# Kernel tuning notes

Measured on AMD Instinct MI355X. Metric: run time of the kernel, lower is better.

Reference implementation:

```python
import jax, jax.numpy as jnp
import numpy as np

N_NODES = 50000
NEG_SLOPE = 0.2


def _gat_layer(h, W, al, ar, src, dst, residual):
    # h: [N, F_in], W: [F_in, H*D], al/ar: [H, D]
    N = h.shape[0]
    H, D = al.shape
    feat = (h @ W).reshape(N, H, D)                      # [N, H, D]
    el = jnp.sum(feat * al[None], axis=-1)               # [N, H]
    er = jnp.sum(feat * ar[None], axis=-1)               # [N, H]
    e = jax.nn.leaky_relu(el[src] + er[dst], NEG_SLOPE)  # [E, H]
    # edge softmax over incoming edges of each destination node
    m = jax.ops.segment_max(e, dst, num_segments=N)      # [N, H]
    m = jnp.where(jnp.isfinite(m), m, jnp.zeros_like(m))
    ex = jnp.exp(e - m[dst])                             # [E, H]
    den = jax.ops.segment_sum(ex, dst, num_segments=N)   # [N, H]
    a = ex / jnp.maximum(den[dst], jnp.asarray(1e-9, ex.dtype))
    msg = a[:, :, None] * feat[src]                      # [E, H, D]
    out = jax.ops.segment_sum(msg, dst, num_segments=N)  # [N, H, D]
    if residual:  # identity residual: in_feats == H*D
        out = out + h.reshape(N, H, D)
    out = jax.nn.relu(out)
    return out.reshape(N, H * D)


def setup_inputs() -> dict:
    key = jax.random.key(0)
    ks = jax.random.split(key, 12)
    N, E, F_IN, H, D = N_NODES, 400000, 256, 4, 64
    s = 1.0 / np.sqrt(F_IN)
    inp = {
        "x": jax.random.normal(ks[0], (N, F_IN), dtype=jnp.float32),
        "src": jax.random.randint(ks[1], (E,), 0, N, dtype=jnp.int32),
        "dst": jax.random.randint(ks[2], (E,), 0, N, dtype=jnp.int32),
    }
    for i in range(3):
        inp[f"W{i}"] = jax.random.normal(ks[3 + 3 * i], (F_IN, H * D), dtype=jnp.float32) * s
        inp[f"al{i}"] = jax.random.normal(ks[4 + 3 * i], (H, D), dtype=jnp.float32) * s
        inp[f"ar{i}"] = jax.random.normal(ks[5 + 3 * i], (H, D), dtype=jnp.float32) * s
    return inp


def reference(x, src, dst, W0, al0, ar0, W1, al1, ar1, W2, al2, ar2):
    h = _gat_layer(x, W0, al0, ar0, src, dst, residual=True)
    h = _gat_layer(h, W1, al1, ar1, src, dst, residual=True)
    h = _gat_layer(h, W2, al2, ar2, src, dst, residual=False)  # last_residual = encoding and residual = False
    return h
```

## Files before the change

### kernel.cpp

```cpp
#include <hip/hip_runtime.h>
#include <stdint.h>

typedef __bf16 bf16x8 __attribute__((ext_vector_type(8)));
typedef float f32x4 __attribute__((ext_vector_type(4)));

typedef __attribute__((address_space(1))) const unsigned int gu32;
typedef __attribute__((address_space(3))) unsigned int lu32;
__device__ __forceinline__ void gl_lds16(const void* g, void* l) {
  __builtin_amdgcn_global_load_lds((gu32*)g, (lu32*)l, 16, 0, 0);
}

__device__ __forceinline__ ushort f2bf(float f) {
  uint32_t u = __float_as_uint(f);
  u += 0x7FFFu + ((u >> 16) & 1u);
  return (ushort)(u >> 16);
}
__device__ __forceinline__ float bflo(uint u) { return __uint_as_float(u << 16); }
__device__ __forceinline__ float bfhi(uint u) { return __uint_as_float(u & 0xFFFF0000u); }

__global__ __launch_bounds__(256) void k_prep(const float* __restrict__ x,
                                              ushort* __restrict__ xb,
                                              const float* __restrict__ W0,
                                              const float* __restrict__ W1,
                                              const float* __restrict__ W2,
                                              ushort* __restrict__ T0,
                                              ushort* __restrict__ T1,
                                              ushort* __restrict__ T2,
                                              const int* __restrict__ dst,
                                              int* __restrict__ cnt,
                                              long totx, int E, int nb_cast) {
  __shared__ float t[64][65];
  int b = blockIdx.x;
  int tid = threadIdx.x;
  if (b < nb_cast) {
    long i = ((long)b * 256 + tid) * 8;
    if (i >= totx) return;
    float4 a = *(const float4*)(x + i);
    float4 c = *(const float4*)(x + i + 4);
    uint4 r;
    r.x = (uint)f2bf(a.x) | ((uint)f2bf(a.y) << 16);
    r.y = (uint)f2bf(a.z) | ((uint)f2bf(a.w) << 16);
    r.z = (uint)f2bf(c.x) | ((uint)f2bf(c.y) << 16);
    r.w = (uint)f2bf(c.z) | ((uint)f2bf(c.w) << 16);
    *(uint4*)(xb + i) = r;
  } else if (b < nb_cast + 48) {
    int idx = b - nb_cast;
    int z = idx >> 4, tile = idx & 15;
    const float* W = z == 0 ? W0 : (z == 1 ? W1 : W2);
    ushort* T = z == 0 ? T0 : (z == 1 ? T1 : T2);
    int r0 = (tile >> 2) * 64, c0 = (tile & 3) * 64;
    int tr = tid >> 4, tc = tid & 15;
#pragma unroll
    for (int i = 0; i < 4; ++i) {
      int r = tr + i * 16;
      float4 v = *(const float4*)(W + (size_t)(r0 + r) * 256 + c0 + tc * 4);
      t[r][tc * 4 + 0] = v.x; t[r][tc * 4 + 1] = v.y;
      t[r][tc * 4 + 2] = v.z; t[r][tc * 4 + 3] = v.w;
    }
    __syncthreads();
#pragma unroll
    for (int i = 0; i < 4; ++i) {
      int nn = tr + i * 16;
      int kk = tc * 4;
      ushort4 o;
      o.x = f2bf(t[kk + 0][nn]); o.y = f2bf(t[kk + 1][nn]);
      o.z = f2bf(t[kk + 2][nn]); o.w = f2bf(t[kk + 3][nn]);
      *(ushort4*)(T + (size_t)(c0 + nn) * 256 + r0 + kk) = o;
    }
  } else {
    int e = (b - nb_cast - 48) * 256 + tid;
    if (e < E) atomicAdd(&cnt[dst[e]], 1);
  }
}

__global__ __launch_bounds__(1024) void k_scan1(const int* __restrict__ cnt,
                                                int* __restrict__ rowptr,
                                                int* __restrict__ bsum, int N) {
  __shared__ int wsum[16];
  int tid = threadIdx.x, lane = tid & 63, wv = tid >> 6;
  int i = blockIdx.x * 1024 + tid;
  int v = (i < N) ? cnt[i] : 0;
  int x = v;
#pragma unroll
  for (int off = 1; off < 64; off <<= 1) {
    int y = __shfl_up(x, off);
    if (lane >= off) x += y;
  }
  if (lane == 63) wsum[wv] = x;
  __syncthreads();
  if (wv == 0) {
    int s = (lane < 16) ? wsum[lane] : 0;
#pragma unroll
    for (int off = 1; off < 16; off <<= 1) {
      int y = __shfl_up(s, off);
      if (lane >= off) s += y;
    }
    if (lane < 16) wsum[lane] = s;
  }
  __syncthreads();
  x += wv ? wsum[wv - 1] : 0;
  if (i < N) rowptr[i + 1] = x;
  if (tid == 0) bsum[blockIdx.x] = wsum[15];
}

__global__ void k_scan2(int* __restrict__ bsum, int G) {
  int lane = threadIdx.x & 63;
  int carry = 0;
  for (int base = 0; base < G; base += 64) {
    int b = base + lane;
    int v = (b < G) ? bsum[b] : 0;
    int x = v;
#pragma unroll
    for (int off = 1; off < 64; off <<= 1) {
      int y = __shfl_up(x, off);
      if (lane >= off) x += y;
    }
    if (b < G) bsum[b] = carry + x - v;
    carry += __shfl(x, 63);
  }
}

__global__ __launch_bounds__(1024) void k_scan3(int* __restrict__ rowptr,
                                                const int* __restrict__ bsum, int N) {
  int i = blockIdx.x * 1024 + threadIdx.x;
  if (i < N) rowptr[i + 1] += bsum[blockIdx.x];
  if (blockIdx.x == 0 && threadIdx.x == 0) rowptr[0] = 0;
}

__global__ __launch_bounds__(256) void k_scatter(const int* __restrict__ dst,
                                                 const int* __restrict__ src,
                                                 const int* __restrict__ rowptr,
                                                 int* __restrict__ fill,
                                                 int* __restrict__ esrc, int E) {
  int e = blockIdx.x * 256 + threadIdx.x;
  if (e < E) {
    int d = dst[e];
    int p = atomicAdd(&fill[d], 1);
    esrc[rowptr[d] + p] = src[e];
  }
}

#define BM 128
#define BN 128
#define BK 64

__global__ __launch_bounds__(512) void k_gemm_bf16(const ushort* __restrict__ A,
                                                   const ushort* __restrict__ Bt,
                                                   const float* __restrict__ al,
                                                   const float* __restrict__ ar,
                                                   ushort* __restrict__ C,
                                                   float* __restrict__ el,
                                                   float* __restrict__ er, int M) {
  __shared__ __align__(16) ushort As[2 * BM * BK];
  __shared__ __align__(16) ushort Bs[2 * BN * BK];
  const int K = 256, N = 256;
  int bn = blockIdx.x * BN;
  int bm = blockIdx.y * BM;
  int tid = threadIdx.x;
  int lane = tid & 63, wid = tid >> 6;
  int wr = wid >> 1;
  int wc = wid & 1;

  f32x4 acc[2][4];
#pragma unroll
  for (int mi = 0; mi < 2; ++mi)
#pragma unroll
    for (int ni = 0; ni < 4; ++ni) acc[mi][ni] = (f32x4){0.f, 0.f, 0.f, 0.f};

  auto stage = [&](int kt, int buf) {
#pragma unroll
    for (int i = 0; i < 2; ++i) {
      int r = i * 64 + (tid >> 3);
      int cs = (((tid & 7) ^ (r & 7)) << 3);
      int gr = bm + r;
      if (gr >= M) gr = M - 1;
      gl_lds16(A + (size_t)gr * K + kt + cs, As + buf * 8192 + i * 4096 + wid * 512);
      gl_lds16(Bt + (size_t)(bn + r) * K + kt + cs, Bs + buf * 8192 + i * 4096 + wid * 512);
    }
  };

  stage(0, 0);
  asm volatile("s_waitcnt vmcnt(0)" ::: "memory");
  __builtin_amdgcn_s_barrier();

  int swz = (lane & 7) << 3;
#pragma unroll
  for (int t = 0; t < 4; ++t) {
    int cur = t & 1;
    if (t < 3) stage((t + 1) * BK, cur ^ 1);
    const ushort* Ab = As + cur * 8192;
    const ushort* Bb = Bs + cur * 8192;
#pragma unroll
    for (int s = 0; s < 2; ++s) {
      bf16x8 af[2], bfr[4];
      int cc = s * 32 + (lane >> 4) * 8;
      int cs = cc ^ swz;
#pragma unroll
      for (int mi = 0; mi < 2; ++mi) {
        int r = wr * 32 + mi * 16 + (lane & 15);
        af[mi] = *(const bf16x8*)(Ab + r * BK + cs);
      }
#pragma unroll
      for (int ni = 0; ni < 4; ++ni) {
        int r = wc * 64 + ni * 16 + (lane & 15);
        bfr[ni] = *(const bf16x8*)(Bb + r * BK + cs);
      }
#pragma unroll
      for (int mi = 0; mi < 2; ++mi)
#pragma unroll
        for (int ni = 0; ni < 4; ++ni)
          acc[mi][ni] = __builtin_amdgcn_mfma_f32_16x16x32_bf16(af[mi], bfr[ni], acc[mi][ni], 0, 0, 0);
    }
    if (t < 3) {
      asm volatile("s_waitcnt vmcnt(0)" ::: "memory");
      __builtin_amdgcn_s_barrier();
    }
  }

#pragma unroll
  for (int mi = 0; mi < 2; ++mi) {
#pragma unroll
    for (int j = 0; j < 4; ++j) {
      int gr = bm + wr * 32 + mi * 16 + (lane >> 4) * 4 + j;
      if (gr < M) {
#pragma unroll
        for (int ni = 0; ni < 4; ++ni) {
          int gc = bn + wc * 64 + ni * 16 + (lane & 15);
          C[(size_t)gr * N + gc] = f2bf(acc[mi][ni][j]);
        }
      }
    }
  }

  int h = (bn >> 6) + wc;
  float alv[4], arv[4];
#pragma unroll
  for (int ni = 0; ni < 4; ++ni) {
    int d = ni * 16 + (lane & 15);
    alv[ni] = al[h * 64 + d];
    arv[ni] = ar[h * 64 + d];
  }
#pragma unroll
  for (int mi = 0; mi < 2; ++mi) {
#pragma unroll
    for (int j = 0; j < 4; ++j) {
      float pel = acc[mi][0][j] * alv[0] + acc[mi][1][j] * alv[1] +
                  acc[mi][2][j] * alv[2] + acc[mi][3][j] * alv[3];
      float per = acc[mi][0][j] * arv[0] + acc[mi][1][j] * arv[1] +
                  acc[mi][2][j] * arv[2] + acc[mi][3][j] * arv[3];
#pragma unroll
      for (int off = 8; off >= 1; off >>= 1) {
        pel += __shfl_xor(pel, off);
        per += __shfl_xor(per, off);
      }
      int gr = bm + wr * 32 + mi * 16 + (lane >> 4) * 4 + j;
      if ((lane & 15) == 0 && gr < M) {
        el[(size_t)gr * 4 + h] = pel;
        er[(size_t)gr * 4 + h] = per;
      }
    }
  }
}

#define CAP 128

__global__ __launch_bounds__(256) void k_agg(const ushort* __restrict__ feat,
                                             const float* __restrict__ el,
                                             const float* __restrict__ er,
                                             const int* __restrict__ rowptr,
                                             const int* __restrict__ esrc,
                                             const float* __restrict__ resid_f32,
                                             const ushort* __restrict__ resid_bf16,
                                             float* __restrict__ out_f32,
                                             ushort* __restrict__ out_bf16, int N) {
  __shared__ float lw[4][CAP * 4];
  int wv = threadIdx.x >> 6;
  int lane = threadIdx.x & 63;
  int n = blockIdx.x * 4 + wv;
  if (n >= N) return;
  int e0 = rowptr[n], e1 = rowptr[n + 1];
  int deg = e1 - e0;
  int h = lane >> 4, sub = lane & 15;
  float ern = er[(size_t)n * 4 + h];
  const ushort* fb = feat + (size_t)lane * 4;

  float a0 = 0.f, a1 = 0.f, a2 = 0.f, a3 = 0.f;
  float inv;

  if (deg <= 16) {
    int s_reg = 0;
    float v = -1e30f;
    if (sub < deg) {
      s_reg = esrc[e0 + sub];
      v = el[(size_t)s_reg * 4 + h] + ern;
      v = v >= 0.f ? v : 0.2f * v;
    }
    float m = v;
    m = fmaxf(m, __shfl_xor(m, 1));
    m = fmaxf(m, __shfl_xor(m, 2));
    m = fmaxf(m, __shfl_xor(m, 4));
    m = fmaxf(m, __shfl_xor(m, 8));
    float w_reg = (sub < deg) ? __expf(v - m) : 0.f;
    float den = w_reg;
    den += __shfl_xor(den, 1);
    den += __shfl_xor(den, 2);
    den += __shfl_xor(den, 4);
    den += __shfl_xor(den, 8);
    inv = 1.f / fmaxf(den, 1e-9f);
    int hb = h << 4;
    int j = 0;
    for (; j + 8 <= deg; j += 8) {
      int s[8];
      uint2 f[8];
      float w[8];
#pragma unroll
      for (int t = 0; t < 8; ++t) s[t] = __shfl(s_reg, j + t);
#pragma unroll
      for (int t = 0; t < 8; ++t) f[t] = *(const uint2*)(fb + (size_t)s[t] * 256);
#pragma unroll
      for (int t = 0; t < 8; ++t) w[t] = __shfl(w_reg, hb + j + t);
#pragma unroll
      for (int t = 0; t < 8; ++t) {
        a0 += w[t] * bflo(f[t].x); a1 += w[t] * bfhi(f[t].x);
        a2 += w[t] * bflo(f[t].y); a3 += w[t] * bfhi(f[t].y);
      }
    }
    if (j + 4 <= deg) {
      int s[4];
      uint2 f[4];
      float w[4];
#pragma unroll
      for (int t = 0; t < 4; ++t) s[t] = __shfl(s_reg, j + t);
#pragma unroll
      for (int t = 0; t < 4; ++t) f[t] = *(const uint2*)(fb + (size_t)s[t] * 256);
#pragma unroll
      for (int t = 0; t < 4; ++t) w[t] = __shfl(w_reg, hb + j + t);
#pragma unroll
      for (int t = 0; t < 4; ++t) {
        a0 += w[t] * bflo(f[t].x); a1 += w[t] * bfhi(f[t].x);
        a2 += w[t] * bflo(f[t].y); a3 += w[t] * bfhi(f[t].y);
      }
      j += 4;
    }
    for (; j < deg; ++j) {
      int sj = __shfl(s_reg, j);
      uint2 f = *(const uint2*)(fb + (size_t)sj * 256);
      float wj = __shfl(w_reg, hb + j);
      a0 += wj * bflo(f.x); a1 += wj * bfhi(f.x); a2 += wj * bflo(f.y); a3 += wj * bfhi(f.y);
    }
  } else {
    float* lwp = lw[wv];
    float m = -1e30f;
    for (int jj = sub; jj < deg; jj += 16) {
      int s = esrc[e0 + jj];
      float v = el[(size_t)s * 4 + h] + ern;
      v = v >= 0.f ? v : 0.2f * v;
      if (jj < CAP) lwp[jj * 4 + h] = v;
      m = fmaxf(m, v);
    }
    m = fmaxf(m, __shfl_xor(m, 1));
    m = fmaxf(m, __shfl_xor(m, 2));
    m = fmaxf(m, __shfl_xor(m, 4));
    m = fmaxf(m, __shfl_xor(m, 8));
    float den = 0.f;
    for (int jj = sub; jj < deg; jj += 16) {
      float v;
      if (jj < CAP) {
        v = lwp[jj * 4 + h];
      } else {
        int s = esrc[e0 + jj];
        v = el[(size_t)s * 4 + h] + ern;
        v = v >= 0.f ? v : 0.2f * v;
      }
      float w = __expf(v - m);
      if (jj < CAP) lwp[jj * 4 + h] = w;
      den += w;
    }
    den += __shfl_xor(den, 1);
    den += __shfl_xor(den, 2);
    den += __shfl_xor(den, 4);
    den += __shfl_xor(den, 8);
    inv = 1.f / fmaxf(den, 1e-9f);

    if (deg <= CAP) {
      int j = 0;
      for (; j + 8 <= deg; j += 8) {
        int s[8];
        uint2 f[8];
        float w[8];
#pragma unroll
        for (int t = 0; t < 8; ++t) s[t] = esrc[e0 + j + t];
#pragma unroll
        for (int t = 0; t < 8; ++t) f[t] = *(const uint2*)(fb + (size_t)s[t] * 256);
#pragma unroll
        for (int t = 0; t < 8; ++t) w[t] = lwp[(j + t) * 4 + h];
#pragma unroll
        for (int t = 0; t < 8; ++t) {
          a0 += w[t] * bflo(f[t].x); a1 += w[t] * bfhi(f[t].x);
          a2 += w[t] * bflo(f[t].y); a3 += w[t] * bfhi(f[t].y);
        }
      }
      for (; j < deg; ++j) {
        int s = esrc[e0 + j];
        uint2 f = *(const uint2*)(fb + (size_t)s * 256);
        float w = lwp[j * 4 + h];
        a0 += w * bflo(f.x); a1 += w * bfhi(f.x); a2 += w * bflo(f.y); a3 += w * bfhi(f.y);
      }
    } else {
      for (int j = 0; j < deg; ++j) {
        int s = esrc[e0 + j];
        float w;
        if (j < CAP) {
          w = lwp[j * 4 + h];
        } else {
          float v = el[(size_t)s * 4 + h] + ern;
          v = v >= 0.f ? v : 0.2f * v;
          w = __expf(v - m);
        }
        uint2 f = *(const uint2*)(fb + (size_t)s * 256);
        a0 += w * bflo(f.x); a1 += w * bfhi(f.x); a2 += w * bflo(f.y); a3 += w * bfhi(f.y);
      }
    }
  }

  float o0 = a0 * inv, o1 = a1 * inv, o2 = a2 * inv, o3 = a3 * inv;
  size_t base = (size_t)n * 256 + lane * 4;
  if (resid_f32) {
    float4 r = *(const float4*)(resid_f32 + base);
    o0 += r.x; o1 += r.y; o2 += r.z; o3 += r.w;
  } else if (resid_bf16) {
    uint2 r = *(const uint2*)(resid_bf16 + base);
    o0 += bflo(r.x); o1 += bfhi(r.x); o2 += bflo(r.y); o3 += bfhi(r.y);
  }
  o0 = fmaxf(o0, 0.f); o1 = fmaxf(o1, 0.f); o2 = fmaxf(o2, 0.f); o3 = fmaxf(o3, 0.f);
  if (out_f32) {
    float4 o = {o0, o1, o2, o3};
    *(float4*)(out_f32 + base) = o;
  }
  if (out_bf16) {
    uint2 p;
    p.x = (uint)f2bf(o0) | ((uint)f2bf(o1) << 16);
    p.y = (uint)f2bf(o2) | ((uint)f2bf(o3) << 16);
    *(uint2*)(out_bf16 + base) = p;
  }
}

extern "C" void kernel_launch(void* const* d_in, const int* in_sizes, int n_in,
                              void* d_out, int out_size, void* d_ws, size_t ws_size,
                              hipStream_t stream) {
  const float* x = (const float*)d_in[0];
  const int* src = (const int*)d_in[1];
  const int* dst = (const int*)d_in[2];
  const float* W[3]  = {(const float*)d_in[3], (const float*)d_in[6], (const float*)d_in[9]};
  const float* al[3] = {(const float*)d_in[4], (const float*)d_in[7], (const float*)d_in[10]};
  const float* ar[3] = {(const float*)d_in[5], (const float*)d_in[8], (const float*)d_in[11]};
  const int N = in_sizes[0] / 256;
  const int E = in_sizes[1];
  float* out = (float*)d_out;

  char* ws = (char*)d_ws;
  size_t off = 0;
  auto alloc = [&](size_t bytes) -> void* {
    void* p = ws + off;
    off += (bytes + 255) & ~(size_t)255;
    return p;
  };
  ushort* xb    = (ushort*)alloc((size_t)N * 256 * 2);
  ushort* h1b   = (ushort*)alloc((size_t)N * 256 * 2);
  ushort* h2b   = (ushort*)alloc((size_t)N * 256 * 2);
  ushort* featb = (ushort*)alloc((size_t)N * 256 * 2);
  float*  el    = (float*)alloc((size_t)N * 4 * 4);
  float*  er    = (float*)alloc((size_t)N * 4 * 4);
  ushort* Wt[3];
  for (int i = 0; i < 3; ++i) Wt[i] = (ushort*)alloc(256 * 256 * 2);
  int* cntfill = (int*)alloc((size_t)N * 2 * 4);
  int* cnt  = cntfill;
  int* fill = cntfill + N;
  int* rowptr = (int*)alloc((size_t)(N + 1) * 4);
  int* esrc   = (int*)alloc((size_t)E * 4);
  int* bsum   = (int*)alloc(4096);

  long totx = (long)N * 256;
  int G = (N + 1023) / 1024;
  int nb_cast = (int)((totx / 8 + 255) / 256);
  int nb_cnt = (E + 255) / 256;

  hipMemsetAsync(cntfill, 0, (size_t)N * 2 * 4, stream);
  k_prep<<<nb_cast + 48 + nb_cnt, 256, 0, stream>>>(x, xb, W[0], W[1], W[2],
                                                    Wt[0], Wt[1], Wt[2], dst, cnt,
                                                    totx, E, nb_cast);
  k_scan1<<<G, 1024, 0, stream>>>(cnt, rowptr, bsum, N);
  k_scan2<<<1, 64, 0, stream>>>(bsum, G);
  k_scan3<<<G, 1024, 0, stream>>>(rowptr, bsum, N);
  k_scatter<<<(E + 255) / 256, 256, 0, stream>>>(dst, src, rowptr, fill, esrc, E);

  dim3 ggrid(2, (N + BM - 1) / BM);
  dim3 agrid((N + 3) / 4);

  k_gemm_bf16<<<ggrid, 512, 0, stream>>>(xb, Wt[0], al[0], ar[0], featb, el, er, N);
  k_agg<<<agrid, 256, 0, stream>>>(featb, el, er, rowptr, esrc, x, nullptr, nullptr, h1b, N);

  k_gemm_bf16<<<ggrid, 512, 0, stream>>>(h1b, Wt[1], al[1], ar[1], featb, el, er, N);
  k_agg<<<agrid, 256, 0, stream>>>(featb, el, er, rowptr, esrc, nullptr, h1b, nullptr, h2b, N);

  k_gemm_bf16<<<ggrid, 512, 0, stream>>>(h2b, Wt[2], al[2], ar[2], featb, el, er, N);
  k_agg<<<agrid, 256, 0, stream>>>(featb, el, er, rowptr, esrc, nullptr, nullptr, out, nullptr, N);
}
```

Before: 254.5 us.

## Switch GEMM to triple-buffered BK=32 pipeline with partial vmcnt waits

Halves the GEMM K-tile to 32 and moves from double to triple buffering in LDS. Loads run two stages ahead, and a partial s_waitcnt vmcnt(2) lets newer loads stay in flight while the current tile is consumed. The swizzle pattern is redone for the narrower rows. LDS use drops from 64KB to 48KB, which may allow more resident blocks, at the cost of twice as many barriers and iterations.

```diff
diff --git a/kernel.cpp b/kernel.cpp
--- a/kernel.cpp
+++ b/kernel.cpp
@@ -142,7 +142,7 @@
 
 #define BM 128
 #define BN 128
-#define BK 64
+#define BK 32
 
 __global__ __launch_bounds__(512) void k_gemm_bf16(const ushort* __restrict__ A,
                                                    const ushort* __restrict__ Bt,
@@ -151,8 +151,8 @@
                                                    ushort* __restrict__ C,
                                                    float* __restrict__ el,
                                                    float* __restrict__ er, int M) {
-  __shared__ __align__(16) ushort As[2 * BM * BK];
-  __shared__ __align__(16) ushort Bs[2 * BN * BK];
+  __shared__ __align__(16) ushort As[3 * BM * BK];
+  __shared__ __align__(16) ushort Bs[3 * BM * BK];
   const int K = 256, N = 256;
   int bn = blockIdx.x * BN;
   int bm = blockIdx.y * BM;
@@ -168,53 +168,46 @@
     for (int ni = 0; ni < 4; ++ni) acc[mi][ni] = (f32x4){0.f, 0.f, 0.f, 0.f};
 
   auto stage = [&](int kt, int buf) {
-#pragma unroll
-    for (int i = 0; i < 2; ++i) {
-      int r = i * 64 + (tid >> 3);
-      int cs = (((tid & 7) ^ (r & 7)) << 3);
-      int gr = bm + r;
-      if (gr >= M) gr = M - 1;
-      gl_lds16(A + (size_t)gr * K + kt + cs, As + buf * 8192 + i * 4096 + wid * 512);
-      gl_lds16(Bt + (size_t)(bn + r) * K + kt + cs, Bs + buf * 8192 + i * 4096 + wid * 512);
-    }
+    int r = tid >> 2;
+    int cs = (((tid & 3) ^ ((r >> 1) & 3)) << 3);
+    int gr = bm + r;
+    if (gr >= M) gr = M - 1;
+    gl_lds16(A + (size_t)gr * K + kt + cs, As + buf * 4096 + wid * 512);
+    gl_lds16(Bt + (size_t)(bn + r) * K + kt + cs, Bs + buf * 4096 + wid * 512);
   };
 
   stage(0, 0);
-  asm volatile("s_waitcnt vmcnt(0)" ::: "memory");
-  __builtin_amdgcn_s_barrier();
-
-  int swz = (lane & 7) << 3;
-#pragma unroll
-  for (int t = 0; t < 4; ++t) {
-    int cur = t & 1;
-    if (t < 3) stage((t + 1) * BK, cur ^ 1);
-    const ushort* Ab = As + cur * 8192;
-    const ushort* Bb = Bs + cur * 8192;
-#pragma unroll
-    for (int s = 0; s < 2; ++s) {
-      bf16x8 af[2], bfr[4];
-      int cc = s * 32 + (lane >> 4) * 8;
-      int cs = cc ^ swz;
-#pragma unroll
-      for (int mi = 0; mi < 2; ++mi) {
-        int r = wr * 32 + mi * 16 + (lane & 15);
-        af[mi] = *(const bf16x8*)(Ab + r * BK + cs);
-      }
-#pragma unroll
-      for (int ni = 0; ni < 4; ++ni) {
-        int r = wc * 64 + ni * 16 + (lane & 15);
-        bfr[ni] = *(const bf16x8*)(Bb + r * BK + cs);
-      }
-#pragma unroll
-      for (int mi = 0; mi < 2; ++mi)
-#pragma unroll
-        for (int ni = 0; ni < 4; ++ni)
-          acc[mi][ni] = __builtin_amdgcn_mfma_f32_16x16x32_bf16(af[mi], bfr[ni], acc[mi][ni], 0, 0, 0);
-    }
-    if (t < 3) {
+  stage(BK, 1);
+
+  int swz = ((lane >> 1) & 3) << 3;
+  int cs = (((lane >> 4) << 3) ^ swz);
+#pragma unroll
+  for (int t = 0; t < 8; ++t) {
+    if (t < 7) {
+      asm volatile("s_waitcnt vmcnt(2)" ::: "memory");
+    } else {
       asm volatile("s_waitcnt vmcnt(0)" ::: "memory");
-      __builtin_amdgcn_s_barrier();
-    }
+    }
+    __builtin_amdgcn_s_barrier();
+    if (t < 6) stage((t + 2) * BK, (t + 2) % 3);
+    const ushort* Ab = As + (t % 3) * 4096;
+    const ushort* Bb = Bs + (t % 3) * 4096;
+    bf16x8 af[2], bfr[4];
+#pragma unroll
+    for (int mi = 0; mi < 2; ++mi) {
+      int r = wr * 32 + mi * 16 + (lane & 15);
+      af[mi] = *(const bf16x8*)(Ab + r * BK + cs);
+    }
+#pragma unroll
+    for (int ni = 0; ni < 4; ++ni) {
+      int r = wc * 64 + ni * 16 + (lane & 15);
+      bfr[ni] = *(const bf16x8*)(Bb + r * BK + cs);
+    }
+#pragma unroll
+    for (int mi = 0; mi < 2; ++mi)
+#pragma unroll
+      for (int ni = 0; ni < 4; ++ni)
+        acc[mi][ni] = __builtin_amdgcn_mfma_f32_16x16x32_bf16(af[mi], bfr[ni], acc[mi][ni], 0, 0, 0);
   }
 
 #pragma unroll
```

After: 253.2 us. About the same (-0.5%).
